# Optimization experiments

Measured on AMD Instinct MI355X. Metric: run time of the kernel, lower is better.

Reference implementation:

```python
import jax, jax.numpy as jnp
import numpy as np

HIDDEN = 4096
N_HEADS = 32
N_KV_HEADS = 8
HEAD_DIM = 128
ROPE_THETA = 1e11
KEY_MULTIPLIER = 0.5
Q_SIZE = N_HEADS * HEAD_DIM
KV_SIZE = N_KV_HEADS * HEAD_DIM
SEQ = 2048


def _rope_neox(x, positions):
    # x: [T, H, D]; neox style: rotate halves of the head dim
    d = x.shape[-1]
    inv_freq = 1.0 / (ROPE_THETA ** (jnp.arange(0, d // 2, dtype=jnp.float32) * (2.0 / d)))
    freqs = positions.astype(jnp.float32)[:, None] * inv_freq[None, :]  # [T, D/2]
    cos = jnp.cos(freqs)[:, None, :]  # [T, 1, D/2]
    sin = jnp.sin(freqs)[:, None, :]
    x1, x2 = x[..., : d // 2], x[..., d // 2 :]
    return jnp.concatenate([x1 * cos - x2 * sin, x2 * cos + x1 * sin], axis=-1)


def setup_inputs() -> dict:
    key = jax.random.key(0)
    k1, k2, k3 = jax.random.split(key, 3)
    scale_in = 1.0 / np.sqrt(HIDDEN)
    return {
        "positions": jnp.arange(SEQ, dtype=jnp.int32),
        "hidden_states": jax.random.normal(k1, (SEQ, HIDDEN), jnp.float32),
        "w_qkv": jax.random.normal(k2, (HIDDEN, Q_SIZE + 2 * KV_SIZE), jnp.float32) * scale_in,
        "w_o": jax.random.normal(k3, (Q_SIZE, HIDDEN), jnp.float32) * scale_in,
    }


def reference(positions, hidden_states, w_qkv, w_o):
    T = hidden_states.shape[0]
    qkv = hidden_states @ w_qkv  # [T, q+2kv]
    q, k, v = jnp.split(qkv, [Q_SIZE, Q_SIZE + KV_SIZE], axis=-1)
    k = k * KEY_MULTIPLIER
    q = q.reshape(T, N_HEADS, HEAD_DIM)
    k = k.reshape(T, N_KV_HEADS, HEAD_DIM)
    v = v.reshape(T, N_KV_HEADS, HEAD_DIM)
    q = _rope_neox(q, positions)
    k = _rope_neox(k, positions)
    # GQA: expand kv heads to query heads
    group = N_HEADS // N_KV_HEADS
    k = jnp.repeat(k, group, axis=1)  # [T, H, D]
    v = jnp.repeat(v, group, axis=1)
    scaling = HEAD_DIM ** -0.5
    scores = jnp.einsum("qhd,khd->hqk", q, k) * scaling  # [H, T, T]
    causal = positions[:, None] >= positions[None, :]  # [T, T]
    scores = jnp.where(causal[None, :, :], scores, jnp.finfo(scores.dtype).min)
    probs = jax.nn.softmax(scores, axis=-1)
    attn = jnp.einsum("hqk,khd->qhd", probs, v).reshape(T, Q_SIZE)
    return attn @ w_o
```

## Files before the change

kernel.cpp:

```cpp
#include <hip/hip_runtime.h>
#include <hip/hip_bf16.h>
#include <math.h>

typedef __bf16 bf16_t;
typedef bf16_t bf16x8 __attribute__((ext_vector_type(8)));
typedef bf16_t bf16x4 __attribute__((ext_vector_type(4)));
typedef float  f32x4  __attribute__((ext_vector_type(4)));

#define HIDDEN 4096
#define NH     32
#define NKV    8
#define HD     128
#define QSZ    4096
#define KVSZ   1024
#define QKVN   6144
#define SEQ    2048
#define ATT_SCALE 0.08838834764831845f
#define KEYMUL 0.5f

static __device__ __forceinline__ void gld_lds16(const void* g, void* l) {
  __builtin_amdgcn_global_load_lds((const __attribute__((address_space(1))) char*)g,
                                   (__attribute__((address_space(3))) char*)l, 16, 0, 0);
}

__global__ __launch_bounds__(256) void cast_f32_bf16(const float* __restrict__ in,
                                                     bf16_t* __restrict__ out) {
  int i = (blockIdx.x * 256 + threadIdx.x) * 4;
  float4 v = *(const float4*)(in + i);
  bf16x4 o;
  o[0] = (bf16_t)v.x; o[1] = (bf16_t)v.y; o[2] = (bf16_t)v.z; o[3] = (bf16_t)v.w;
  *(bf16x4*)(out + i) = o;
}

__global__ __launch_bounds__(256) void transpose_cast(const float* __restrict__ W,
                                                      bf16_t* __restrict__ WT,
                                                      int K, int N) {
  __shared__ float t[32][33];
  int k0 = blockIdx.y * 32, n0 = blockIdx.x * 32;
  int c = threadIdx.x & 31, r = threadIdx.x >> 5;
#pragma unroll
  for (int rr = r; rr < 32; rr += 8)
    t[rr][c] = W[(size_t)(k0 + rr) * N + n0 + c];
  __syncthreads();
#pragma unroll
  for (int rr = r; rr < 32; rr += 8)
    WT[(size_t)(n0 + rr) * K + k0 + c] = (bf16_t)t[c][rr];
}

__global__ __launch_bounds__(256) void vprep(const float* __restrict__ qkv,
                                             bf16_t* __restrict__ VT) {
  __shared__ float t[32][33];
  int h = blockIdx.z;
  int s0 = blockIdx.x * 32, d0 = blockIdx.y * 32;
  int c = threadIdx.x & 31, r = threadIdx.x >> 5;
#pragma unroll
  for (int rr = r; rr < 32; rr += 8)
    t[rr][c] = qkv[(size_t)(s0 + rr) * QKVN + QSZ + KVSZ + h * HD + d0 + c];
  __syncthreads();
#pragma unroll
  for (int rr = r; rr < 32; rr += 8)
    VT[((size_t)h * HD + d0 + rr) * SEQ + s0 + c] = (bf16_t)t[c][rr];
}

__global__ __launch_bounds__(256) void rope_qk(const float* __restrict__ qkv,
                                               const int* __restrict__ positions,
                                               bf16_t* __restrict__ Qh,
                                               bf16_t* __restrict__ Kh) {
  int s = blockIdx.x;
  float pos = (float)positions[s];
  for (int p = threadIdx.x; p < (NH + NKV) * 64; p += 256) {
    int i = p & 63;
    float inv = powf(100000000000.0f, -(float)i * (1.0f / 64.0f));
    float fr = pos * inv;
    float cs = cosf(fr), sn = sinf(fr);
    if (p < NH * 64) {
      int hh = p >> 6;
      const float* base = qkv + (size_t)s * QKVN + hh * HD;
      float x1 = base[i], x2 = base[i + 64];
      bf16_t* ob = Qh + ((size_t)hh * SEQ + s) * HD;
      ob[i]      = (bf16_t)(x1 * cs - x2 * sn);
      ob[i + 64] = (bf16_t)(x2 * cs + x1 * sn);
    } else {
      int hh = (p - NH * 64) >> 6;
      const float* base = qkv + (size_t)s * QKVN + QSZ + hh * HD;
      float x1 = base[i], x2 = base[i + 64];
      bf16_t* ob = Kh + ((size_t)hh * SEQ + s) * HD;
      ob[i]      = (bf16_t)((x1 * cs - x2 * sn) * KEYMUL);
      ob[i + 64] = (bf16_t)((x2 * cs + x1 * sn) * KEYMUL);
    }
  }
}

__global__ __launch_bounds__(256) void gemm_bf16_bt(const bf16_t* __restrict__ A,
                                                    const bf16_t* __restrict__ BT,
                                                    float* __restrict__ C,
                                                    int M, int N, int K) {
  __shared__ __align__(16) bf16_t lA[128 * 32];
  __shared__ __align__(16) bf16_t lB[128 * 32];
  int tid = threadIdx.x;
  int w = tid >> 6, lane = tid & 63;
  int l16 = lane & 15, lhi = lane >> 4;
  int bm = blockIdx.y, bn = blockIdx.x;
  int wm = (w >> 1) * 64, wn = (w & 1) * 64;
  int rowA0 = bm * 128, rowB0 = bn * 128;
  f32x4 acc[4][4] = {};
  int c0 = w * 128 + lane;
  int c1 = c0 + 64;
  const bf16_t* Asrc0 = A + (size_t)(rowA0 + (c0 >> 2)) * K + (c0 & 3) * 8;
  const bf16_t* Asrc1 = A + (size_t)(rowA0 + (c1 >> 2)) * K + (c1 & 3) * 8;
  const bf16_t* Bsrc0 = BT + (size_t)(rowB0 + (c0 >> 2)) * K + (c0 & 3) * 8;
  const bf16_t* Bsrc1 = BT + (size_t)(rowB0 + (c1 >> 2)) * K + (c1 & 3) * 8;

  for (int kt = 0; kt < K; kt += 32) {
    gld_lds16(Asrc0 + kt, lA + c0 * 8);
    gld_lds16(Asrc1 + kt, lA + c1 * 8);
    gld_lds16(Bsrc0 + kt, lB + c0 * 8);
    gld_lds16(Bsrc1 + kt, lB + c1 * 8);
    __syncthreads();
    bf16x8 af[4], bfr[4];
#pragma unroll
    for (int m = 0; m < 4; ++m)
      af[m] = *(const bf16x8*)(lA + (wm + m * 16 + l16) * 32 + lhi * 8);
#pragma unroll
    for (int n = 0; n < 4; ++n)
      bfr[n] = *(const bf16x8*)(lB + (wn + n * 16 + l16) * 32 + lhi * 8);
#pragma unroll
    for (int m = 0; m < 4; ++m)
#pragma unroll
      for (int n = 0; n < 4; ++n)
        acc[m][n] = __builtin_amdgcn_mfma_f32_16x16x32_bf16(af[m], bfr[n], acc[m][n], 0, 0, 0);
    __syncthreads();
  }
#pragma unroll
  for (int m = 0; m < 4; ++m) {
    int row = rowA0 + wm + m * 16 + lhi * 4;
#pragma unroll
    for (int n = 0; n < 4; ++n) {
      int col = rowB0 + wn + n * 16 + l16;
#pragma unroll
      for (int j = 0; j < 4; ++j)
        C[(size_t)(row + j) * N + col] = acc[m][n][j];
    }
  }
}

__global__ __launch_bounds__(256) void attn_kernel(const bf16_t* __restrict__ Q,
                                                   const bf16_t* __restrict__ Kb,
                                                   const bf16_t* __restrict__ VT,
                                                   bf16_t* __restrict__ Oa) {
  __shared__ __align__(16) char KV[2][2][16384];
  __shared__ __align__(16) bf16_t Plds[4][16][72];
  int h = blockIdx.y, p = blockIdx.x;
  int kvh = h >> 2;
  int tid = threadIdx.x;
  int w = tid >> 6, lane = tid & 63;
  int l16 = lane & 15, lhi = lane >> 4;
  int xr = (l16 & 7) << 4;

  int kRow[4], kCol[4], vRow[4], vCol[4], ldsOff[4];
#pragma unroll
  for (int i = 0; i < 4; ++i) {
    int X = w * 4096 + i * 1024 + lane * 16;
    ldsOff[i] = X;
    kRow[i] = X >> 8;
    kCol[i] = (X & 255) ^ ((kRow[i] & 7) << 4);
    vRow[i] = X >> 7;
    vCol[i] = (X & 127) ^ ((vRow[i] & 7) << 4);
  }
  const char* Kg = (const char*)(Kb + (size_t)kvh * SEQ * HD);
  const char* Vg = (const char*)(VT + (size_t)kvh * HD * SEQ);

  int qts[2] = {p, 31 - p};
  int nts[2] = {p + 1, 32 - p};

  for (int ph = 0; ph < 2; ++ph) {
    int qt = qts[ph], ntile = nts[ph];
    int qrow0 = qt * 64 + w * 16;

    bf16x8 qf[4];
    const bf16_t* qbase = Q + ((size_t)h * SEQ + qrow0 + l16) * HD;
#pragma unroll
    for (int kk = 0; kk < 4; ++kk)
      qf[kk] = *(const bf16x8*)(qbase + kk * 32 + lhi * 8);

    f32x4 o[8] = {};
    float m_r[4], l_r[4];
#pragma unroll
    for (int j = 0; j < 4; ++j) { m_r[j] = -1e30f; l_r[j] = 0.0f; }

#pragma unroll
    for (int i = 0; i < 4; ++i) {
      gld_lds16(Kg + (size_t)(0 + kRow[i]) * 256 + kCol[i], &KV[0][0][0] + ldsOff[i]);
      gld_lds16(Vg + (size_t)vRow[i] * (SEQ * 2) + 0 + vCol[i], &KV[0][1][0] + ldsOff[i]);
    }
    __syncthreads();

    for (int kt = 0; kt < ntile; ++kt) {
      int b = kt & 1;
      int kb = kt * 64;
      if (kt + 1 < ntile) {
        int kb2 = kb + 64;
#pragma unroll
        for (int i = 0; i < 4; ++i) {
          gld_lds16(Kg + (size_t)(kb2 + kRow[i]) * 256 + kCol[i], &KV[b ^ 1][0][0] + ldsOff[i]);
          gld_lds16(Vg + (size_t)vRow[i] * (SEQ * 2) + (size_t)kb2 * 2 + vCol[i], &KV[b ^ 1][1][0] + ldsOff[i]);
        }
      }
      const char* Kl = &KV[b][0][0];
      const char* Vl = &KV[b][1][0];

      f32x4 s4[4] = {};
#pragma unroll
      for (int n = 0; n < 4; ++n) {
        int r = n * 16 + l16;
#pragma unroll
        for (int kk = 0; kk < 4; ++kk) {
          bf16x8 kf = *(const bf16x8*)(Kl + r * 256 + ((kk * 64 + lhi * 16) ^ xr));
          s4[n] = __builtin_amdgcn_mfma_f32_16x16x32_bf16(qf[kk], kf, s4[n], 0, 0, 0);
        }
      }
      float pv[4][4];
#pragma unroll
      for (int n = 0; n < 4; ++n) {
        int col = kb + n * 16 + l16;
#pragma unroll
        for (int j = 0; j < 4; ++j) {
          int row = qrow0 + lhi * 4 + j;
          float v = s4[n][j] * ATT_SCALE;
          pv[n][j] = (col > row) ? -1e30f : v;
        }
      }
      float mx[4];
#pragma unroll
      for (int j = 0; j < 4; ++j) {
        mx[j] = fmaxf(fmaxf(pv[0][j], pv[1][j]), fmaxf(pv[2][j], pv[3][j]));
#pragma unroll
        for (int d = 1; d < 16; d <<= 1)
          mx[j] = fmaxf(mx[j], __shfl_xor(mx[j], d));
      }
      float mn[4], sc[4], rs[4];
#pragma unroll
      for (int j = 0; j < 4; ++j) {
        mn[j] = fmaxf(m_r[j], mx[j]);
        sc[j] = __expf(m_r[j] - mn[j]);
        m_r[j] = mn[j];
      }
#pragma unroll
      for (int n = 0; n < 4; ++n)
#pragma unroll
        for (int j = 0; j < 4; ++j)
          pv[n][j] = __expf(pv[n][j] - mn[j]);
#pragma unroll
      for (int j = 0; j < 4; ++j) {
        rs[j] = pv[0][j] + pv[1][j] + pv[2][j] + pv[3][j];
#pragma unroll
        for (int d = 1; d < 16; d <<= 1)
          rs[j] += __shfl_xor(rs[j], d);
        l_r[j] = l_r[j] * sc[j] + rs[j];
      }
#pragma unroll
      for (int nf = 0; nf < 8; ++nf)
#pragma unroll
        for (int j = 0; j < 4; ++j)
          o[nf][j] *= sc[j];
#pragma unroll
      for (int n = 0; n < 4; ++n)
#pragma unroll
        for (int j = 0; j < 4; ++j)
          Plds[w][lhi * 4 + j][n * 16 + l16] = (bf16_t)pv[n][j];
#pragma unroll
      for (int ks = 0; ks < 2; ++ks) {
        bf16x8 pa = *(const bf16x8*)&Plds[w][l16][ks * 32 + lhi * 8];
#pragma unroll
        for (int nf = 0; nf < 8; ++nf) {
          int d = nf * 16 + l16;
          bf16x8 vf = *(const bf16x8*)(Vl + d * 128 + ((ks * 64 + lhi * 16) ^ xr));
          o[nf] = __builtin_amdgcn_mfma_f32_16x16x32_bf16(pa, vf, o[nf], 0, 0, 0);
        }
      }
      __syncthreads();
    }
#pragma unroll
    for (int j = 0; j < 4; ++j) {
      float inv_l = 1.0f / l_r[j];
      int row = qrow0 + lhi * 4 + j;
#pragma unroll
      for (int nf = 0; nf < 8; ++nf)
        Oa[(size_t)row * QSZ + h * HD + nf * 16 + l16] = (bf16_t)(o[nf][j] * inv_l);
    }
    __syncthreads();
  }
}

extern "C" void kernel_launch(void* const* d_in, const int* in_sizes, int n_in,
                              void* d_out, int out_size, void* d_ws, size_t ws_size,
                              hipStream_t stream) {
  const int*   positions = (const int*)d_in[0];
  const float* hidden    = (const float*)d_in[1];
  const float* w_qkv     = (const float*)d_in[2];
  const float* w_o       = (const float*)d_in[3];
  float* out = (float*)d_out;

  char* ws = (char*)d_ws;
  size_t off = 0;
  auto alloc = [&](size_t bytes) { void* p = ws + off; off += (bytes + 255) & ~255ULL; return p; };
  bf16_t* h_bf  = (bf16_t*)alloc((size_t)SEQ * HIDDEN * 2);
  bf16_t* wqkvT = (bf16_t*)alloc((size_t)QKVN * HIDDEN * 2);
  bf16_t* woT   = (bf16_t*)alloc((size_t)HIDDEN * QSZ * 2);
  float*  qkv   = (float*)alloc((size_t)SEQ * QKVN * 4);
  bf16_t* Qh    = (bf16_t*)alloc((size_t)NH * SEQ * HD * 2);
  bf16_t* Kh    = (bf16_t*)alloc((size_t)NKV * SEQ * HD * 2);
  bf16_t* VT    = (bf16_t*)alloc((size_t)NKV * HD * SEQ * 2);
  bf16_t* Oa    = (bf16_t*)alloc((size_t)SEQ * QSZ * 2);
  (void)ws_size; (void)in_sizes; (void)n_in; (void)out_size;

  cast_f32_bf16<<<SEQ * HIDDEN / 4 / 256, 256, 0, stream>>>(hidden, h_bf);
  transpose_cast<<<dim3(QKVN / 32, HIDDEN / 32), 256, 0, stream>>>(w_qkv, wqkvT, HIDDEN, QKVN);
  transpose_cast<<<dim3(HIDDEN / 32, QSZ / 32), 256, 0, stream>>>(w_o, woT, QSZ, HIDDEN);
  gemm_bf16_bt<<<dim3(QKVN / 128, SEQ / 128), 256, 0, stream>>>(h_bf, wqkvT, qkv, SEQ, QKVN, HIDDEN);
  rope_qk<<<SEQ, 256, 0, stream>>>(qkv, positions, Qh, Kh);
  vprep<<<dim3(SEQ / 32, HD / 32, NKV), 256, 0, stream>>>(qkv, VT);
  attn_kernel<<<dim3(16, NH), 256, 0, stream>>>(Qh, Kh, VT, Oa);
  gemm_bf16_bt<<<dim3(HIDDEN / 128, SEQ / 128), 256, 0, stream>>>(Oa, woT, out, SEQ, HIDDEN, QSZ);
}
```

Measured before the change: 601.5 us.

## Replace GEMM with 256x256-tile double-buffered kernel using swizzled LDS

Both projection GEMMs move from a 128x128, single-buffered, 256-thread kernel to a 512-thread kernel with 256x256 output tiles and a K-step of 64. It prefetches two stages ahead into double-buffered LDS using direct global-to-LDS loads and explicit vmcnt waits. LDS rows are XOR-swizzled to avoid bank conflicts, block IDs are remapped for L2 locality, and s_setprio is raised around the MFMA bursts. The larger tiles cut global and LDS traffic per FLOP. In exchange, only 192 and 128 workgroups are launched, so fewer blocks than CUs may leave part of the GPU idle, and the 128 KB of LDS limits occupancy.

```diff
diff --git a/kernel.cpp b/kernel.cpp
--- a/kernel.cpp
+++ b/kernel.cpp
@@ -91,52 +91,99 @@
   }
 }
 
-__global__ __launch_bounds__(256) void gemm_bf16_bt(const bf16_t* __restrict__ A,
-                                                    const bf16_t* __restrict__ BT,
-                                                    float* __restrict__ C,
-                                                    int M, int N, int K) {
-  __shared__ __align__(16) bf16_t lA[128 * 32];
-  __shared__ __align__(16) bf16_t lB[128 * 32];
-  int tid = threadIdx.x;
-  int w = tid >> 6, lane = tid & 63;
-  int l16 = lane & 15, lhi = lane >> 4;
-  int bm = blockIdx.y, bn = blockIdx.x;
-  int wm = (w >> 1) * 64, wn = (w & 1) * 64;
-  int rowA0 = bm * 128, rowB0 = bn * 128;
-  f32x4 acc[4][4] = {};
-  int c0 = w * 128 + lane;
-  int c1 = c0 + 64;
-  const bf16_t* Asrc0 = A + (size_t)(rowA0 + (c0 >> 2)) * K + (c0 & 3) * 8;
-  const bf16_t* Asrc1 = A + (size_t)(rowA0 + (c1 >> 2)) * K + (c1 & 3) * 8;
-  const bf16_t* Bsrc0 = BT + (size_t)(rowB0 + (c0 >> 2)) * K + (c0 & 3) * 8;
-  const bf16_t* Bsrc1 = BT + (size_t)(rowB0 + (c1 >> 2)) * K + (c1 & 3) * 8;
-
-  for (int kt = 0; kt < K; kt += 32) {
-    gld_lds16(Asrc0 + kt, lA + c0 * 8);
-    gld_lds16(Asrc1 + kt, lA + c1 * 8);
-    gld_lds16(Bsrc0 + kt, lB + c0 * 8);
-    gld_lds16(Bsrc1 + kt, lB + c1 * 8);
-    __syncthreads();
-    bf16x8 af[4], bfr[4];
-#pragma unroll
-    for (int m = 0; m < 4; ++m)
-      af[m] = *(const bf16x8*)(lA + (wm + m * 16 + l16) * 32 + lhi * 8);
+__global__ __launch_bounds__(512, 2) void gemm256(const bf16_t* __restrict__ A,
+                                                  const bf16_t* __restrict__ BT,
+                                                  float* __restrict__ C,
+                                                  int M, int N, int K) {
+  __shared__ __align__(16) bf16_t lA[2][256 * 64];
+  __shared__ __align__(16) bf16_t lB[2][256 * 64];
+  const int tid = threadIdx.x;
+  const int w = tid >> 6, lane = tid & 63, l16 = lane & 15, lhi = lane >> 4;
+  const int wm2 = w >> 2, wn4 = w & 3;
+
+  const int nbx = N >> 8;
+  const int nwg = nbx * (M >> 8);
+  int bid = blockIdx.x;
+  int swz = (bid & 7) * (nwg >> 3) + (bid >> 3);
+  const int bm = swz / nbx, bn = swz % nbx;
+
+  const int NT = K >> 6;
+
+  int sRow[4], sCol[4];
+#pragma unroll
+  for (int i = 0; i < 4; ++i) {
+    int X = i * 8192 + tid * 16;
+    sRow[i] = X >> 7;
+    sCol[i] = (X & 127) ^ ((sRow[i] & 7) << 4);
+  }
+  const char* Ag = (const char*)(A + (size_t)bm * 256 * K);
+  const char* Bg = (const char*)(BT + (size_t)bn * 256 * K);
+
+  auto stage = [&](int t, int buf) {
+#pragma unroll
+    for (int i = 0; i < 4; ++i)
+      gld_lds16(Ag + (size_t)sRow[i] * (K * 2) + t * 128 + sCol[i],
+                (char*)&lA[buf][0] + i * 8192 + tid * 16);
+#pragma unroll
+    for (int i = 0; i < 4; ++i)
+      gld_lds16(Bg + (size_t)sRow[i] * (K * 2) + t * 128 + sCol[i],
+                (char*)&lB[buf][0] + i * 8192 + tid * 16);
+  };
+
+  f32x4 acc[8][4] = {};
+  stage(0, 0);
+  stage(1, 1);
+
+  for (int t = 0; t < NT; ++t) {
+    const int cur = t & 1;
+    if (t == NT - 1) asm volatile("s_waitcnt vmcnt(0)" ::: "memory");
+    else             asm volatile("s_waitcnt vmcnt(8)" ::: "memory");
+    __builtin_amdgcn_s_barrier();
+    asm volatile("" ::: "memory");
+    const char* Ab = (const char*)&lA[cur][0];
+    const char* Bb = (const char*)&lB[cur][0];
+
+    bf16x8 bF[4][2];
 #pragma unroll
     for (int n = 0; n < 4; ++n)
-      bfr[n] = *(const bf16x8*)(lB + (wn + n * 16 + l16) * 32 + lhi * 8);
-#pragma unroll
-    for (int m = 0; m < 4; ++m)
-#pragma unroll
-      for (int n = 0; n < 4; ++n)
-        acc[m][n] = __builtin_amdgcn_mfma_f32_16x16x32_bf16(af[m], bfr[n], acc[m][n], 0, 0, 0);
-    __syncthreads();
-  }
-#pragma unroll
-  for (int m = 0; m < 4; ++m) {
-    int row = rowA0 + wm + m * 16 + lhi * 4;
+#pragma unroll
+      for (int ks = 0; ks < 2; ++ks) {
+        int row = wn4 * 64 + n * 16 + l16;
+        bF[n][ks] = *(const bf16x8*)(Bb + row * 128 + ((ks * 64 + lhi * 16) ^ ((row & 7) << 4)));
+      }
+#pragma unroll
+    for (int q = 0; q < 4; ++q) {
+      bf16x8 aF[2][2];
+#pragma unroll
+      for (int mi = 0; mi < 2; ++mi)
+#pragma unroll
+        for (int ks = 0; ks < 2; ++ks) {
+          int row = wm2 * 128 + (q * 2 + mi) * 16 + l16;
+          aF[mi][ks] = *(const bf16x8*)(Ab + row * 128 + ((ks * 64 + lhi * 16) ^ ((row & 7) << 4)));
+        }
+      __builtin_amdgcn_s_setprio(1);
+#pragma unroll
+      for (int mi = 0; mi < 2; ++mi)
+#pragma unroll
+        for (int n = 0; n < 4; ++n)
+#pragma unroll
+          for (int ks = 0; ks < 2; ++ks)
+            acc[q * 2 + mi][n] = __builtin_amdgcn_mfma_f32_16x16x32_bf16(
+                aF[mi][ks], bF[n][ks], acc[q * 2 + mi][n], 0, 0, 0);
+      __builtin_amdgcn_s_setprio(0);
+    }
+    asm volatile("" ::: "memory");
+    __builtin_amdgcn_s_barrier();
+    asm volatile("" ::: "memory");
+    if (t + 2 < NT) stage(t + 2, cur);
+  }
+
+#pragma unroll
+  for (int m = 0; m < 8; ++m) {
+    int row = bm * 256 + wm2 * 128 + m * 16 + lhi * 4;
 #pragma unroll
     for (int n = 0; n < 4; ++n) {
-      int col = rowB0 + wn + n * 16 + l16;
+      int col = bn * 256 + wn4 * 64 + n * 16 + l16;
 #pragma unroll
       for (int j = 0; j < 4; ++j)
         C[(size_t)(row + j) * N + col] = acc[m][n][j];
@@ -317,9 +364,9 @@
   cast_f32_bf16<<<SEQ * HIDDEN / 4 / 256, 256, 0, stream>>>(hidden, h_bf);
   transpose_cast<<<dim3(QKVN / 32, HIDDEN / 32), 256, 0, stream>>>(w_qkv, wqkvT, HIDDEN, QKVN);
   transpose_cast<<<dim3(HIDDEN / 32, QSZ / 32), 256, 0, stream>>>(w_o, woT, QSZ, HIDDEN);
-  gemm_bf16_bt<<<dim3(QKVN / 128, SEQ / 128), 256, 0, stream>>>(h_bf, wqkvT, qkv, SEQ, QKVN, HIDDEN);
+  gemm256<<<(SEQ / 256) * (QKVN / 256), 512, 0, stream>>>(h_bf, wqkvT, qkv, SEQ, QKVN, HIDDEN);
   rope_qk<<<SEQ, 256, 0, stream>>>(qkv, positions, Qh, Kh);
   vprep<<<dim3(SEQ / 32, HD / 32, NKV), 256, 0, stream>>>(qkv, VT);
   attn_kernel<<<dim3(16, NH), 256, 0, stream>>>(Qh, Kh, VT, Oa);
-  gemm_bf16_bt<<<dim3(HIDDEN / 128, SEQ / 128), 256, 0, stream>>>(Oa, woT, out, SEQ, HIDDEN, QSZ);
-}
+  gemm256<<<(SEQ / 256) * (HIDDEN / 256), 512, 0, stream>>>(Oa, woT, out, SEQ, HIDDEN, QSZ);
+}
```

Measured after the change: 639.5 us. +6.3%, slower.
